# Performance work log

Measured on AMD Instinct MI355X. Metric: run time of the kernel, lower is better.

## Reference

```python
import jax, jax.numpy as jnp
import numpy as np

B, N, U, H = 4, 4096, 256, 4
NEG_PAD = -(2.0 ** 32) + 1.0  # paddings value from torch code


def setup_inputs() -> dict:
    key = jax.random.key(0)
    k1, k2, k3, k4 = jax.random.split(key, 4)
    return {
        "x": jax.random.normal(k1, (B, N, U), dtype=jnp.float32),
        "input_mask": jnp.zeros((B, N), dtype=bool),
        "Wq": jax.random.normal(k2, (U, U), dtype=jnp.float32) * 0.02,
        "Wk": jax.random.normal(k3, (U, U), dtype=jnp.float32) * 0.02,
        "Wv": jax.random.normal(k4, (U, U), dtype=jnp.float32) * 0.02,
    }


def reference(x, input_mask, Wq, Wk, Wv):
    b, n, u = x.shape
    h = H
    dh = u // h
    scale = 1.0 / np.sqrt(dh).astype(np.float32)

    # nn.Linear(bias=False): y = x @ W.T ; head split via split(dim=2)+cat(dim=0)
    # == reshape (b,n,h,dh) then move head to front -> (h,b,n,dh)
    def proj(W):
        return (x @ W.T).reshape(b, n, h, dh).transpose(2, 0, 1, 3)

    Q = proj(Wq)  # (h,b,n,dh)
    K = proj(Wk)
    V = proj(Wv)

    scores = jnp.einsum('hbqd,hbkd->hbqk', Q, K) * scale  # (h,b,n,n)

    # key mask: zero-norm keys get huge negative score
    key_masks = jnp.sign(jnp.sum(jnp.abs(K), axis=-1))  # (h,b,n)
    scores = jnp.where(key_masks[:, :, None, :] == 0, NEG_PAD, scores)

    # directional mask: attention_mask[i,j] = (j > i) for FORWARD (meshgrid ij,
    # sw_col=i, sw_row=j, greater(sw_row, sw_col)); adder kills mask==False
    idx = jnp.arange(n)
    dir_mask = idx[None, :] > idx[:, None]  # (n,n) strict upper triangle
    scores = scores + (1.0 - dir_mask.astype(scores.dtype)) * -10000.0

    attn = jax.nn.softmax(scores, axis=-1)

    # post-softmax query mask
    query_masks = jnp.sign(jnp.sum(jnp.abs(Q), axis=-1))  # (h,b,n)
    attn = attn * query_masks[..., None]

    # dropout p=0.0 -> identity
    out = jnp.einsum('hbqk,hbkd->hbqd', attn, V)  # (h,b,n,dh)
    # recombine heads: split(dim=0)+cat(dim=2) inverse -> (b,n,u)
    out = out.transpose(1, 2, 0, 3).reshape(b, n, u)

    # output value masking with ~input_mask
    out = out * (~input_mask)[..., None].astype(out.dtype)
    return out
```

## Files before the change

kernel.cpp:

```cpp
#include <hip/hip_runtime.h>
#include <hip/hip_bf16.h>
#include <stdint.h>


#define BB 4
#define NNQ 4096
#define UU 256
#define DHE 64
#define NPAIR 16
#define QBLK 128
#define KVB 128
#define NT (NNQ / KVB)
#define BIAS2 (-14426.950408889634f)
#define QSCALE 0.1803368801111244f

typedef __attribute__((ext_vector_type(8))) short bf16x8;
typedef __attribute__((ext_vector_type(4))) float f32x4;
typedef __attribute__((ext_vector_type(16))) float f32x16;
typedef unsigned short u16;
typedef unsigned int u32;

typedef __attribute__((address_space(3))) void lds_t;
typedef const __attribute__((address_space(1))) void glb_t;

__device__ __forceinline__ u16 f2bf(float f) {
    union { float f; unsigned u; } v; v.f = f;
    unsigned r = v.u + 0x7fffu + ((v.u >> 16) & 1u);
    return (u16)(r >> 16);
}

__device__ __forceinline__ float bf2f(u16 h) {
    union { unsigned u; float f; } v; v.u = ((unsigned)h) << 16;
    return v.f;
}

__device__ __forceinline__ bf16x8 load_cvt8(const float* p) {
    const float4* q = (const float4*)p;
    float4 a = q[0], b = q[1];
    bf16x8 r;
    r[0] = (short)f2bf(a.x); r[1] = (short)f2bf(a.y);
    r[2] = (short)f2bf(a.z); r[3] = (short)f2bf(a.w);
    r[4] = (short)f2bf(b.x); r[5] = (short)f2bf(b.y);
    r[6] = (short)f2bf(b.z); r[7] = (short)f2bf(b.w);
    return r;
}

__device__ __forceinline__ void gload16(const void* g, void* l) {
    __builtin_amdgcn_global_load_lds((glb_t*)g, (lds_t*)l, 16, 0, 0);
}

__device__ __forceinline__ float exp2_hw(float x) {
    float r;
    asm("v_exp_f32 %0, %1" : "=v"(r) : "v"(x));
    return r;
}

__device__ __forceinline__ float max3_hw(float a, float b, float c) {
    float r;
    asm("v_max3_f32 %0, %1, %2, %3" : "=v"(r) : "v"(a), "v"(b), "v"(c));
    return r;
}

__device__ __forceinline__ u32 cvt_pk_bf16(float a, float b) {
    u32 r;
    asm("v_cvt_pk_bf16_f32 %0, %1, %2" : "=v"(r) : "v"(a), "v"(b));
    return r;
}

__device__ __forceinline__ void pswap(u32& a, u32& b) {
    asm volatile("v_permlane32_swap_b32 %0, %1" : "+v"(a), "+v"(b));
}

__global__ __launch_bounds__(256) void cvt_kernel(
    const float* __restrict__ x, const float* __restrict__ Wq,
    const float* __restrict__ Wk, const float* __restrict__ Wv,
    u16* __restrict__ xb, u16* __restrict__ Wb)
{
    const int bx = blockIdx.x;
    if (bx < 2048) {
        const int i = (bx * 256 + threadIdx.x) * 8;
        *(bf16x8*)&xb[i] = load_cvt8(&x[i]);
    } else {
        const int zz = (bx - 2048) >> 5;
        const float* src = (zz == 0) ? Wq : (zz == 1) ? Wk : Wv;
        const int i = ((((bx - 2048) & 31) * 256) + threadIdx.x) * 8;
        *(bf16x8*)&Wb[zz * 65536 + i] = load_cvt8(&src[i]);
    }
}

__global__ __launch_bounds__(256) void proj_kernel(
    const u16* __restrict__ xb, const u16* __restrict__ Wb,
    u16* __restrict__ Qb, u16* __restrict__ Kb, u16* __restrict__ Vt)
{
    __shared__ __align__(16) u16 xbuf[64 * 256];

    const int tid = threadIdx.x;
    const int l = tid & 63;
    const int w = tid >> 6;
    const int l15 = l & 15;
    const int g = l >> 4;
    const int g8 = g * 8;
    const int z = blockIdx.y;
    const u16* W = Wb + (size_t)z * 65536;
    const int mbase = blockIdx.x * 64;

#pragma unroll
    for (int i = 0; i < 8; i++) {
        int D = tid * 16 + i * 4096;
        int S = D ^ (((D >> 9) & 7) << 4);
        gload16(xb + (size_t)mbase * UU + (S >> 1), xbuf + (D >> 1));
    }

    f32x4 acc[4][4];
#pragma unroll
    for (int mt = 0; mt < 4; mt++)
#pragma unroll
        for (int j = 0; j < 4; j++) acc[mt][j] = (f32x4){0.f, 0.f, 0.f, 0.f};

    __syncthreads();

#pragma unroll
    for (int kb = 0; kb < UU; kb += 32) {
        bf16x8 wf[4];
#pragma unroll
        for (int j = 0; j < 4; j++)
            wf[j] = *(const bf16x8*)&W[(size_t)(w * 64 + j * 16 + l15) * UU + kb + g8];
        bf16x8 af[4];
#pragma unroll
        for (int mt = 0; mt < 4; mt++) {
            int row = mt * 16 + l15;
            int A = row * 512 + (kb + g8) * 2;
            A ^= (row & 7) << 4;
            af[mt] = *(const bf16x8*)((const char*)xbuf + A);
        }
#pragma unroll
        for (int mt = 0; mt < 4; mt++)
#pragma unroll
            for (int j = 0; j < 4; j++)
                acc[mt][j] = __builtin_amdgcn_mfma_f32_16x16x32_bf16(af[mt], wf[j], acc[mt][j], 0, 0, 0);
    }

    __syncthreads();
    u16* vt = xbuf;
    const float scale = (z == 0) ? QSCALE : 1.0f;
#pragma unroll
    for (int mt = 0; mt < 4; mt++)
#pragma unroll
        for (int j = 0; j < 4; j++)
#pragma unroll
            for (int r = 0; r < 4; r++)
                vt[w * 4096 + (mt * 16 + g * 4 + r) * 64 + j * 16 + l15] =
                    f2bf(acc[mt][j][r] * scale);
    __syncthreads();

    const int bq = mbase >> 12;
    const int nbase = mbase & (NNQ - 1);
    if (z < 2) {
        u16* dst = (z == 0) ? Qb : Kb;
        const int row = tid >> 2, c16 = (tid & 3) * 16;
#pragma unroll
        for (int h = 0; h < 4; h++) {
            const int pair = h * BB + bq;
            uint4 v0 = *(const uint4*)&vt[h * 4096 + row * 64 + c16];
            uint4 v1 = *(const uint4*)&vt[h * 4096 + row * 64 + c16 + 8];
            uint4* outp = (uint4*)&dst[((size_t)pair * NNQ + nbase + row) * DHE + c16];
            outp[0] = v0; outp[1] = v1;
        }
    } else {
        const int d = tid >> 2, qq = tid & 3;
#pragma unroll
        for (int h = 0; h < 4; h++) {
            const int pair = h * BB + bq;
            u16 vals[16];
#pragma unroll
            for (int e = 0; e < 16; e++) vals[e] = vt[h * 4096 + (qq * 16 + e) * 64 + d];
            unsigned uu0[8];
#pragma unroll
            for (int e = 0; e < 8; e++)
                uu0[e] = (unsigned)vals[2 * e] | ((unsigned)vals[2 * e + 1] << 16);
            uint4* outp = (uint4*)&Vt[((size_t)(pair * DHE + d)) * NNQ + nbase + qq * 16];
            outp[0] = (uint4){uu0[0], uu0[1], uu0[2], uu0[3]};
            outp[1] = (uint4){uu0[4], uu0[5], uu0[6], uu0[7]};
        }
    }
}

__device__ __forceinline__ void stage_kv(u16* kd, u16* vd,
                                         const u16* Kp, const u16* Vp,
                                         int t, int tid)
{
#pragma unroll
    for (int i = 0; i < 2; i++) {
        int off_b = tid * 16 + i * 8192;
        int ks = off_b ^ (((off_b >> 7) & 7) << 4);
        gload16(Kp + (size_t)t * (KVB * DHE) + (ks >> 1), kd + tid * 8 + i * 4096);
        int vs = off_b ^ (((off_b >> 8) & 15) << 4);
        int d = vs >> 8;
        int c = (vs & 255) >> 1;
        gload16(Vp + (size_t)d * NNQ + t * KVB + c, vd + tid * 8 + i * 4096);
    }
}

__global__ __launch_bounds__(512, 4) void attn_kernel(
    const u16* __restrict__ Qb, const u16* __restrict__ Kb,
    const u16* __restrict__ Vt, float* __restrict__ out)
{
    __shared__ __align__(16) u16 kbuf[2][KVB * DHE];
    __shared__ __align__(16) u16 vbuf[2][DHE * KVB];
    __shared__ float mls[4][2][64];

    const int tid = threadIdx.x;
    const int l = tid & 63;
    const int w = tid >> 6;
    const int wq = w & 3;
    const int wk = w >> 2;
    const int l31 = l & 31;
    const int hi = l >> 5;
    const int hi8 = hi * 8;

    const int b = blockIdx.x;
    const int pair = (b & 7) | ((b >> 8) << 3);
    int b3 = (b >> 3) & 31;
    if (b >= 256) b3 = 31 - b3;
    const int qi = b3;
    const int qb = qi * QBLK;
    const int t0 = qi;

    const u16* Kp = Kb + (size_t)pair * NNQ * DHE;
    const u16* Vp = Vt + (size_t)pair * DHE * NNQ;

    stage_kv(kbuf[0], vbuf[0], Kp, Vp, t0, tid);

    const int wrow = qb + wq * 32;
    const int iq = wrow + l31;
    bf16x8 qf[4];
#pragma unroll
    for (int ds = 0; ds < 4; ds++)
        qf[ds] = *(const bf16x8*)&Qb[((size_t)pair * NNQ + iq) * DHE + ds * 16 + hi8];

    f32x16 oaccT[2];
#pragma unroll
    for (int dg = 0; dg < 2; dg++)
#pragma unroll
        for (int r = 0; r < 16; r++) oaccT[dg][r] = 0.f;
    float mrow = -1e30f;
    float lrow = 0.f;

    int cur = 0;
    for (int t = t0; t < NT; ++t) {
        __syncthreads();
        if (t + 1 < NT) stage_kv(kbuf[cur ^ 1], vbuf[cur ^ 1], Kp, Vp, t + 1, tid);

        const u16* kb_ = kbuf[cur];
        const u16* vb_ = vbuf[cur];

        f32x16 sT[2];
#pragma unroll
        for (int kg = 0; kg < 2; kg++)
#pragma unroll
            for (int r = 0; r < 16; r++) sT[kg][r] = 0.f;

        __builtin_amdgcn_s_setprio(1);
#pragma unroll
        for (int kg = 0; kg < 2; kg++)
#pragma unroll
            for (int ds = 0; ds < 4; ds++) {
                int e = (wk * 64 + kg * 32 + l31) * DHE + ds * 16 + hi8;
                e ^= ((e >> 6) & 7) << 3;
                bf16x8 kf = *(const bf16x8*)&kb_[e];
                sT[kg] = __builtin_amdgcn_mfma_f32_32x32x16_bf16(kf, qf[ds], sT[kg], 0, 0, 0);
            }
        __builtin_amdgcn_s_setprio(0);

        if (t == qi) {
#pragma unroll
            for (int kg = 0; kg < 2; kg++)
#pragma unroll
                for (int r = 0; r < 16; r++) {
                    int j = t * KVB + wk * 64 + kg * 32 + (r & 3) + 8 * (r >> 2) + 4 * hi;
                    if (j <= iq) sT[kg][r] += BIAS2;
                }
        }

        {
            float pmk[2];
#pragma unroll
            for (int kg = 0; kg < 2; kg++) {
                float v0 = max3_hw(sT[kg][0], sT[kg][1], sT[kg][2]);
                float v1 = max3_hw(sT[kg][3], sT[kg][4], sT[kg][5]);
                float v2 = max3_hw(sT[kg][6], sT[kg][7], sT[kg][8]);
                float v3 = max3_hw(sT[kg][9], sT[kg][10], sT[kg][11]);
                float v4 = max3_hw(sT[kg][12], sT[kg][13], sT[kg][14]);
                pmk[kg] = max3_hw(max3_hw(v0, v1, v2), fmaxf(v3, v4), sT[kg][15]);
            }
            float pm = fmaxf(pmk[0], pmk[1]);
            pm = fmaxf(pm, __shfl_xor(pm, 32));
            if (!__all(pm <= mrow + 8.0f)) {
                float mn = fmaxf(mrow, pm);
                float f = exp2_hw(mrow - mn);
                mrow = mn;
                lrow *= f;
                oaccT[0] *= f;
                oaccT[1] *= f;
            }
            float rs = 0.f;
#pragma unroll
            for (int kg = 0; kg < 2; kg++) {
#pragma unroll
                for (int r = 0; r < 16; r++)
                    sT[kg][r] = exp2_hw(sT[kg][r] - mrow);
                float s0 = (sT[kg][0] + sT[kg][1]) + (sT[kg][2] + sT[kg][3]);
                float s1 = (sT[kg][4] + sT[kg][5]) + (sT[kg][6] + sT[kg][7]);
                float s2 = (sT[kg][8] + sT[kg][9]) + (sT[kg][10] + sT[kg][11]);
                float s3 = (sT[kg][12] + sT[kg][13]) + (sT[kg][14] + sT[kg][15]);
                rs += (s0 + s1) + (s2 + s3);
            }
            rs += __shfl_xor(rs, 32);
            lrow += rs;
        }

        __builtin_amdgcn_s_setprio(1);
#pragma unroll
        for (int kg = 0; kg < 2; kg++) {
            u32 wv[8];
#pragma unroll
            for (int i = 0; i < 8; i++)
                wv[i] = cvt_pk_bf16(sT[kg][2 * i], sT[kg][2 * i + 1]);
            pswap(wv[0], wv[2]); pswap(wv[1], wv[3]);
            pswap(wv[4], wv[6]); pswap(wv[5], wv[7]);
#pragma unroll
            for (int ks = 0; ks < 2; ks++) {
                union { uint4 u; bf16x8 v; } pk;
                pk.u = (uint4){wv[ks * 4 + 0], wv[ks * 4 + 1],
                               wv[ks * 4 + 2], wv[ks * 4 + 3]};
                const int ksg = kg * 2 + ks;
#pragma unroll
                for (int dg = 0; dg < 2; dg++) {
                    int e = (dg * 32 + l31) * KVB + wk * 64 + ksg * 16 + hi8;
                    e ^= ((e >> 7) & 15) << 3;
                    bf16x8 vf = *(const bf16x8*)&vb_[e];
                    oaccT[dg] = __builtin_amdgcn_mfma_f32_32x32x16_bf16(vf, pk.v, oaccT[dg], 0, 0, 0);
                }
            }
        }
        __builtin_amdgcn_s_setprio(0);
        cur ^= 1;
    }

    __syncthreads();
    float* mb = (float*)&kbuf[0][0];
    if (wk == 1) {
        float* base = mb + wq * 2048;
#pragma unroll
        for (int dg = 0; dg < 2; dg++)
#pragma unroll
            for (int r = 0; r < 16; r++)
                base[(dg * 16 + r) * 64 + l] = oaccT[dg][r];
        mls[wq][0][l] = mrow;
        mls[wq][1][l] = lrow;
    }
    __syncthreads();
    if (wk == 0) {
        const float m1 = mls[wq][0][l];
        const float l1 = mls[wq][1][l];
        const float mn = fmaxf(mrow, m1);
        float f0 = exp2_hw(mrow - mn);
        float f1 = exp2_hw(m1 - mn);
        const float inv = 1.0f / (lrow * f0 + l1 * f1);
        f0 *= inv; f1 *= inv;
        const float* base = mb + wq * 2048;
        const int hh = pair >> 2, bb2 = pair & 3;
        float* op = &out[((size_t)(bb2 * NNQ + iq)) * UU + hh * DHE];
#pragma unroll
        for (int dg = 0; dg < 2; dg++)
#pragma unroll
            for (int rg = 0; rg < 4; rg++) {
                float vv[4];
#pragma unroll
                for (int q4 = 0; q4 < 4; q4++) {
                    int r = rg * 4 + q4;
                    vv[q4] = oaccT[dg][r] * f0 + base[(dg * 16 + r) * 64 + l] * f1;
                }
                *(float4*)&op[dg * 32 + rg * 8 + hi * 4] =
                    (float4){vv[0], vv[1], vv[2], vv[3]};
            }
    }
}

__global__ __launch_bounds__(256) void fixA_kernel(
    const u16* __restrict__ Qb, const u16* __restrict__ Kb,
    const u16* __restrict__ Vt, float* __restrict__ part)
{
    __shared__ float qs[DHE];
    __shared__ float pls[256];
    __shared__ float red[256];
    __shared__ float r4[8];

    const int tid = threadIdx.x;
    const int wv = tid >> 6;
    const int pair = blockIdx.x;
    const int sl = blockIdx.y;

    if (tid < 8) {
        bf16x8 v = *(const bf16x8*)&Qb[((size_t)pair * NNQ + (NNQ - 1)) * DHE + tid * 8];
#pragma unroll
        for (int e = 0; e < 8; e++) qs[tid * 8 + e] = bf2f((u16)v[e]);
    }
    __syncthreads();

    const int j = sl * 256 + tid;
    const u16* kr = Kb + ((size_t)pair * NNQ + j) * DHE;
    float acc = 0.f;
#pragma unroll
    for (int i = 0; i < 8; i++) {
        bf16x8 kv = *(const bf16x8*)&kr[i * 8];
#pragma unroll
        for (int e = 0; e < 8; e++) acc += qs[i * 8 + e] * bf2f((u16)kv[e]);
    }

    float m = acc;
#pragma unroll
    for (int d2 = 1; d2 < 64; d2 <<= 1) m = fmaxf(m, __shfl_xor(m, d2));
    if ((tid & 63) == 0) r4[wv] = m;
    __syncthreads();
    const float gm = fmaxf(fmaxf(r4[0], r4[1]), fmaxf(r4[2], r4[3]));

    const float p = exp2_hw(acc - gm);
    pls[tid] = p;
    float s = p;
#pragma unroll
    for (int d2 = 1; d2 < 64; d2 <<= 1) s += __shfl_xor(s, d2);
    if ((tid & 63) == 0) r4[4 + wv] = s;
    __syncthreads();
    const float gs = (r4[4] + r4[5]) + (r4[6] + r4[7]);

    const int d = tid & 63;
    const int qq = tid >> 6;
    const u16* vrow = Vt + ((size_t)pair * DHE + d) * NNQ + sl * 256 + qq * 64;
    float o = 0.f;
#pragma unroll
    for (int jj = 0; jj < 64; jj += 8) {
        bf16x8 vvv = *(const bf16x8*)&vrow[jj];
#pragma unroll
        for (int e = 0; e < 8; e++) o += pls[qq * 64 + jj + e] * bf2f((u16)vvv[e]);
    }
    red[tid] = o;
    __syncthreads();
    if (tid < 64) {
        float oo = (red[tid] + red[tid + 64]) + (red[tid + 128] + red[tid + 192]);
        float* pp = part + ((size_t)pair * 16 + sl) * 66;
        if (tid == 0) { pp[0] = gm; pp[1] = gs; }
        pp[2 + tid] = oo;
    }
}

__global__ __launch_bounds__(64) void fixB_kernel(
    const float* __restrict__ part, float* __restrict__ out)
{
    const int pair = blockIdx.x;
    const int d = threadIdx.x;
    float gm = -1e30f;
#pragma unroll
    for (int i = 0; i < 16; i++)
        gm = fmaxf(gm, part[((size_t)pair * 16 + i) * 66]);
    float gs = 0.f, od = 0.f;
#pragma unroll
    for (int i = 0; i < 16; i++) {
        const float* pp = &part[((size_t)pair * 16 + i) * 66];
        float wgt = exp2_hw(pp[0] - gm);
        gs += pp[1] * wgt;
        od += pp[2 + d] * wgt;
    }
    const int hh = pair >> 2, bb2 = pair & 3;
    out[((size_t)(bb2 * NNQ + (NNQ - 1))) * UU + hh * DHE + d] = od / gs;
}

extern "C" void kernel_launch(void* const* d_in, const int* in_sizes, int n_in,
                              void* d_out, int out_size, void* d_ws, size_t ws_size,
                              hipStream_t stream)
{
    const float* x  = (const float*)d_in[0];
    const float* Wq = (const float*)d_in[2];
    const float* Wk = (const float*)d_in[3];
    const float* Wv = (const float*)d_in[4];
    float* out = (float*)d_out;

    u16* Qb = (u16*)d_ws;
    u16* Kb = Qb + (size_t)NPAIR * NNQ * DHE;
    u16* Vt = Kb + (size_t)NPAIR * NNQ * DHE;
    float* part = (float*)(Vt + (size_t)NPAIR * DHE * NNQ);

    u16* Wb = (u16*)d_out;
    u16* xb = (u16*)d_out + 262144;

    cvt_kernel<<<2144, 256, 0, stream>>>(x, Wq, Wk, Wv, xb, Wb);

    dim3 pgrid(256, 3);
    proj_kernel<<<pgrid, 256, 0, stream>>>(xb, Wb, Qb, Kb, Vt);

    attn_kernel<<<512, 512, 0, stream>>>(Qb, Kb, Vt, out);

    dim3 fgrid(16, 16);
    fixA_kernel<<<fgrid, 256, 0, stream>>>(Qb, Kb, Vt, part);
    fixB_kernel<<<16, 64, 0, stream>>>(part, out);
}
```

Before: 96.28 us.

## Split long causal query blocks across two workgroups and fuse x conversion into projection

The attention work is rebalanced. Query blocks 0-15 have the longest key ranges, so each is split into two key-range halves handled by different workgroups. Those workgroups write bf16 partial outputs with their max and sum, and a new merge kernel combines them. The second-half workgroups also process the short query blocks 16-31 directly, so every workgroup does about 17 tiles. Separately, the x-to-bf16 conversion is folded into proj_kernel's LDS fill, which removes a pass over x. The cost is an extra launch, partial-buffer traffic, and bf16 rounding of the partial outputs.

```diff
diff --git a/kernel.cpp b/kernel.cpp
--- a/kernel.cpp
+++ b/kernel.cpp
@@ -10,7 +10,7 @@
 #define NPAIR 16
 #define QBLK 128
 #define KVB 128
-#define NT (NNQ / KVB)
+#define NT 32
 #define BIAS2 (-14426.950408889634f)
 #define QSCALE 0.1803368801111244f
 
@@ -71,25 +71,18 @@
     asm volatile("v_permlane32_swap_b32 %0, %1" : "+v"(a), "+v"(b));
 }
 
-__global__ __launch_bounds__(256) void cvt_kernel(
-    const float* __restrict__ x, const float* __restrict__ Wq,
-    const float* __restrict__ Wk, const float* __restrict__ Wv,
-    u16* __restrict__ xb, u16* __restrict__ Wb)
-{
-    const int bx = blockIdx.x;
-    if (bx < 2048) {
-        const int i = (bx * 256 + threadIdx.x) * 8;
-        *(bf16x8*)&xb[i] = load_cvt8(&x[i]);
-    } else {
-        const int zz = (bx - 2048) >> 5;
-        const float* src = (zz == 0) ? Wq : (zz == 1) ? Wk : Wv;
-        const int i = ((((bx - 2048) & 31) * 256) + threadIdx.x) * 8;
-        *(bf16x8*)&Wb[zz * 65536 + i] = load_cvt8(&src[i]);
-    }
+__global__ __launch_bounds__(256) void cvtw_kernel(
+    const float* __restrict__ Wq, const float* __restrict__ Wk,
+    const float* __restrict__ Wv, u16* __restrict__ Wb)
+{
+    const int z = blockIdx.y;
+    const float* src = (z == 0) ? Wq : (z == 1) ? Wk : Wv;
+    const int i = (blockIdx.x * 256 + threadIdx.x) * 8;
+    *(bf16x8*)&Wb[z * 65536 + i] = load_cvt8(&src[i]);
 }
 
 __global__ __launch_bounds__(256) void proj_kernel(
-    const u16* __restrict__ xb, const u16* __restrict__ Wb,
+    const float* __restrict__ x, const u16* __restrict__ Wb,
     u16* __restrict__ Qb, u16* __restrict__ Kb, u16* __restrict__ Vt)
 {
     __shared__ __align__(16) u16 xbuf[64 * 256];
@@ -104,11 +97,16 @@
     const u16* W = Wb + (size_t)z * 65536;
     const int mbase = blockIdx.x * 64;
 
-#pragma unroll
-    for (int i = 0; i < 8; i++) {
-        int D = tid * 16 + i * 4096;
-        int S = D ^ (((D >> 9) & 7) << 4);
-        gload16(xb + (size_t)mbase * UU + (S >> 1), xbuf + (D >> 1));
+    const float4* xs = (const float4*)&x[(size_t)mbase * UU];
+#pragma unroll
+    for (int i = 0; i < 16; i++) {
+        int idx4 = i * 256 + tid;
+        float4 v = xs[idx4];
+        u32 p0 = cvt_pk_bf16(v.x, v.y);
+        u32 p1 = cvt_pk_bf16(v.z, v.w);
+        int Lin = idx4 * 8;
+        int Dst = Lin ^ (((Lin >> 9) & 7) << 4);
+        *(uint2*)((char*)xbuf + Dst) = (uint2){p0, p1};
     }
 
     f32x4 acc[4][4];
@@ -203,7 +201,9 @@
 
 __global__ __launch_bounds__(512, 4) void attn_kernel(
     const u16* __restrict__ Qb, const u16* __restrict__ Kb,
-    const u16* __restrict__ Vt, float* __restrict__ out)
+    const u16* __restrict__ Vt, float* __restrict__ out,
+    float2* __restrict__ pm_a, u16* __restrict__ po_a,
+    float2* __restrict__ pm_b, u16* __restrict__ po_b)
 {
     __shared__ __align__(16) u16 kbuf[2][KVB * DHE];
     __shared__ __align__(16) u16 vbuf[2][DHE * KVB];
@@ -220,171 +220,272 @@
 
     const int b = blockIdx.x;
     const int pair = (b & 7) | ((b >> 8) << 3);
-    int b3 = (b >> 3) & 31;
-    if (b >= 256) b3 = 31 - b3;
-    const int qi = b3;
-    const int qb = qi * QBLK;
-    const int t0 = qi;
+    const int s = (b >> 3) & 31;
+    const int x = s & 15;
+    const int half = s >> 4;
 
     const u16* Kp = Kb + (size_t)pair * NNQ * DHE;
     const u16* Vp = Vt + (size_t)pair * DHE * NNQ;
 
-    stage_kv(kbuf[0], vbuf[0], Kp, Vp, t0, tid);
-
-    const int wrow = qb + wq * 32;
-    const int iq = wrow + l31;
-    bf16x8 qf[4];
-#pragma unroll
-    for (int ds = 0; ds < 4; ds++)
-        qf[ds] = *(const bf16x8*)&Qb[((size_t)pair * NNQ + iq) * DHE + ds * 16 + hi8];
-
     f32x16 oaccT[2];
-#pragma unroll
-    for (int dg = 0; dg < 2; dg++)
-#pragma unroll
-        for (int r = 0; r < 16; r++) oaccT[dg][r] = 0.f;
-    float mrow = -1e30f;
-    float lrow = 0.f;
-
-    int cur = 0;
-    for (int t = t0; t < NT; ++t) {
-        __syncthreads();
-        if (t + 1 < NT) stage_kv(kbuf[cur ^ 1], vbuf[cur ^ 1], Kp, Vp, t + 1, tid);
-
-        const u16* kb_ = kbuf[cur];
-        const u16* vb_ = vbuf[cur];
-
-        f32x16 sT[2];
-#pragma unroll
-        for (int kg = 0; kg < 2; kg++)
-#pragma unroll
-            for (int r = 0; r < 16; r++) sT[kg][r] = 0.f;
-
-        __builtin_amdgcn_s_setprio(1);
-#pragma unroll
-        for (int kg = 0; kg < 2; kg++)
-#pragma unroll
-            for (int ds = 0; ds < 4; ds++) {
-                int e = (wk * 64 + kg * 32 + l31) * DHE + ds * 16 + hi8;
-                e ^= ((e >> 6) & 7) << 3;
-                bf16x8 kf = *(const bf16x8*)&kb_[e];
-                sT[kg] = __builtin_amdgcn_mfma_f32_32x32x16_bf16(kf, qf[ds], sT[kg], 0, 0, 0);
+    float mrow, lrow;
+
+    auto reset = [&]() {
+#pragma unroll
+        for (int dg = 0; dg < 2; dg++)
+#pragma unroll
+            for (int r = 0; r < 16; r++) oaccT[dg][r] = 0.f;
+        mrow = -1e30f; lrow = 0.f;
+    };
+
+    auto flash_pass = [&](int qi, int ta, int tb, bool masked) {
+        if (ta >= tb) return;
+        const int iq = qi * QBLK + wq * 32 + l31;
+        bf16x8 qf[4];
+#pragma unroll
+        for (int ds = 0; ds < 4; ds++)
+            qf[ds] = *(const bf16x8*)&Qb[((size_t)pair * NNQ + iq) * DHE + ds * 16 + hi8];
+
+        stage_kv(kbuf[0], vbuf[0], Kp, Vp, ta, tid);
+        int cur = 0;
+        for (int t = ta; t < tb; ++t) {
+            __syncthreads();
+            if (t + 1 < tb) stage_kv(kbuf[cur ^ 1], vbuf[cur ^ 1], Kp, Vp, t + 1, tid);
+
+            const u16* kb_ = kbuf[cur];
+            const u16* vb_ = vbuf[cur];
+
+            f32x16 sT[2];
+#pragma unroll
+            for (int kg = 0; kg < 2; kg++)
+#pragma unroll
+                for (int r = 0; r < 16; r++) sT[kg][r] = 0.f;
+
+            __builtin_amdgcn_s_setprio(1);
+#pragma unroll
+            for (int kg = 0; kg < 2; kg++)
+#pragma unroll
+                for (int ds = 0; ds < 4; ds++) {
+                    int e = (wk * 64 + kg * 32 + l31) * DHE + ds * 16 + hi8;
+                    e ^= ((e >> 6) & 7) << 3;
+                    bf16x8 kf = *(const bf16x8*)&kb_[e];
+                    sT[kg] = __builtin_amdgcn_mfma_f32_32x32x16_bf16(kf, qf[ds], sT[kg], 0, 0, 0);
+                }
+            __builtin_amdgcn_s_setprio(0);
+
+            if (masked && t == qi) {
+#pragma unroll
+                for (int kg = 0; kg < 2; kg++)
+#pragma unroll
+                    for (int r = 0; r < 16; r++) {
+                        int j = t * KVB + wk * 64 + kg * 32 + (r & 3) + 8 * (r >> 2) + 4 * hi;
+                        if (j <= iq) sT[kg][r] += BIAS2;
+                    }
             }
-        __builtin_amdgcn_s_setprio(0);
-
-        if (t == qi) {
-#pragma unroll
-            for (int kg = 0; kg < 2; kg++)
-#pragma unroll
-                for (int r = 0; r < 16; r++) {
-                    int j = t * KVB + wk * 64 + kg * 32 + (r & 3) + 8 * (r >> 2) + 4 * hi;
-                    if (j <= iq) sT[kg][r] += BIAS2;
+
+            {
+                float pmk[2];
+#pragma unroll
+                for (int kg = 0; kg < 2; kg++) {
+                    float v0 = max3_hw(sT[kg][0], sT[kg][1], sT[kg][2]);
+                    float v1 = max3_hw(sT[kg][3], sT[kg][4], sT[kg][5]);
+                    float v2 = max3_hw(sT[kg][6], sT[kg][7], sT[kg][8]);
+                    float v3 = max3_hw(sT[kg][9], sT[kg][10], sT[kg][11]);
+                    float v4 = max3_hw(sT[kg][12], sT[kg][13], sT[kg][14]);
+                    pmk[kg] = max3_hw(max3_hw(v0, v1, v2), fmaxf(v3, v4), sT[kg][15]);
                 }
-        }
-
-        {
-            float pmk[2];
+                float pm = fmaxf(pmk[0], pmk[1]);
+                pm = fmaxf(pm, __shfl_xor(pm, 32));
+                if (!__all(pm <= mrow + 8.0f)) {
+                    float mn = fmaxf(mrow, pm);
+                    float f = exp2_hw(mrow - mn);
+                    mrow = mn;
+                    lrow *= f;
+                    oaccT[0] *= f;
+                    oaccT[1] *= f;
+                }
+                float rs = 0.f;
+#pragma unroll
+                for (int kg = 0; kg < 2; kg++) {
+#pragma unroll
+                    for (int r = 0; r < 16; r++)
+                        sT[kg][r] = exp2_hw(sT[kg][r] - mrow);
+                    float s0 = (sT[kg][0] + sT[kg][1]) + (sT[kg][2] + sT[kg][3]);
+                    float s1 = (sT[kg][4] + sT[kg][5]) + (sT[kg][6] + sT[kg][7]);
+                    float s2 = (sT[kg][8] + sT[kg][9]) + (sT[kg][10] + sT[kg][11]);
+                    float s3 = (sT[kg][12] + sT[kg][13]) + (sT[kg][14] + sT[kg][15]);
+                    rs += (s0 + s1) + (s2 + s3);
+                }
+                rs += __shfl_xor(rs, 32);
+                lrow += rs;
+            }
+
+            __builtin_amdgcn_s_setprio(1);
 #pragma unroll
             for (int kg = 0; kg < 2; kg++) {
-                float v0 = max3_hw(sT[kg][0], sT[kg][1], sT[kg][2]);
-                float v1 = max3_hw(sT[kg][3], sT[kg][4], sT[kg][5]);
-                float v2 = max3_hw(sT[kg][6], sT[kg][7], sT[kg][8]);
-                float v3 = max3_hw(sT[kg][9], sT[kg][10], sT[kg][11]);
-                float v4 = max3_hw(sT[kg][12], sT[kg][13], sT[kg][14]);
-                pmk[kg] = max3_hw(max3_hw(v0, v1, v2), fmaxf(v3, v4), sT[kg][15]);
-            }
-            float pm = fmaxf(pmk[0], pmk[1]);
-            pm = fmaxf(pm, __shfl_xor(pm, 32));
-            if (!__all(pm <= mrow + 8.0f)) {
-                float mn = fmaxf(mrow, pm);
-                float f = exp2_hw(mrow - mn);
-                mrow = mn;
-                lrow *= f;
-                oaccT[0] *= f;
-                oaccT[1] *= f;
-            }
-            float rs = 0.f;
-#pragma unroll
-            for (int kg = 0; kg < 2; kg++) {
-#pragma unroll
-                for (int r = 0; r < 16; r++)
-                    sT[kg][r] = exp2_hw(sT[kg][r] - mrow);
-                float s0 = (sT[kg][0] + sT[kg][1]) + (sT[kg][2] + sT[kg][3]);
-                float s1 = (sT[kg][4] + sT[kg][5]) + (sT[kg][6] + sT[kg][7]);
-                float s2 = (sT[kg][8] + sT[kg][9]) + (sT[kg][10] + sT[kg][11]);
-                float s3 = (sT[kg][12] + sT[kg][13]) + (sT[kg][14] + sT[kg][15]);
-                rs += (s0 + s1) + (s2 + s3);
-            }
-            rs += __shfl_xor(rs, 32);
-            lrow += rs;
-        }
-
-        __builtin_amdgcn_s_setprio(1);
-#pragma unroll
-        for (int kg = 0; kg < 2; kg++) {
-            u32 wv[8];
-#pragma unroll
-            for (int i = 0; i < 8; i++)
-                wv[i] = cvt_pk_bf16(sT[kg][2 * i], sT[kg][2 * i + 1]);
-            pswap(wv[0], wv[2]); pswap(wv[1], wv[3]);
-            pswap(wv[4], wv[6]); pswap(wv[5], wv[7]);
-#pragma unroll
-            for (int ks = 0; ks < 2; ks++) {
-                union { uint4 u; bf16x8 v; } pk;
-                pk.u = (uint4){wv[ks * 4 + 0], wv[ks * 4 + 1],
-                               wv[ks * 4 + 2], wv[ks * 4 + 3]};
-                const int ksg = kg * 2 + ks;
-#pragma unroll
-                for (int dg = 0; dg < 2; dg++) {
-                    int e = (dg * 32 + l31) * KVB + wk * 64 + ksg * 16 + hi8;
-                    e ^= ((e >> 7) & 15) << 3;
-                    bf16x8 vf = *(const bf16x8*)&vb_[e];
-                    oaccT[dg] = __builtin_amdgcn_mfma_f32_32x32x16_bf16(vf, pk.v, oaccT[dg], 0, 0, 0);
+                u32 wv[8];
+#pragma unroll
+                for (int i = 0; i < 8; i++)
+                    wv[i] = cvt_pk_bf16(sT[kg][2 * i], sT[kg][2 * i + 1]);
+                pswap(wv[0], wv[2]); pswap(wv[1], wv[3]);
+                pswap(wv[4], wv[6]); pswap(wv[5], wv[7]);
+#pragma unroll
+                for (int ks = 0; ks < 2; ks++) {
+                    union { uint4 u; bf16x8 v; } pk;
+                    pk.u = (uint4){wv[ks * 4 + 0], wv[ks * 4 + 1],
+                                   wv[ks * 4 + 2], wv[ks * 4 + 3]};
+                    const int ksg = kg * 2 + ks;
+#pragma unroll
+                    for (int dg = 0; dg < 2; dg++) {
+                        int e = (dg * 32 + l31) * KVB + wk * 64 + ksg * 16 + hi8;
+                        e ^= ((e >> 7) & 15) << 3;
+                        bf16x8 vf = *(const bf16x8*)&vb_[e];
+                        oaccT[dg] = __builtin_amdgcn_mfma_f32_32x32x16_bf16(vf, pk.v, oaccT[dg], 0, 0, 0);
+                    }
                 }
             }
-        }
-        __builtin_amdgcn_s_setprio(0);
-        cur ^= 1;
-    }
-
-    __syncthreads();
-    float* mb = (float*)&kbuf[0][0];
-    if (wk == 1) {
-        float* base = mb + wq * 2048;
-#pragma unroll
-        for (int dg = 0; dg < 2; dg++)
-#pragma unroll
-            for (int r = 0; r < 16; r++)
-                base[(dg * 16 + r) * 64 + l] = oaccT[dg][r];
-        mls[wq][0][l] = mrow;
-        mls[wq][1][l] = lrow;
-    }
-    __syncthreads();
-    if (wk == 0) {
-        const float m1 = mls[wq][0][l];
-        const float l1 = mls[wq][1][l];
-        const float mn = fmaxf(mrow, m1);
-        float f0 = exp2_hw(mrow - mn);
-        float f1 = exp2_hw(m1 - mn);
-        const float inv = 1.0f / (lrow * f0 + l1 * f1);
-        f0 *= inv; f1 *= inv;
-        const float* base = mb + wq * 2048;
-        const int hh = pair >> 2, bb2 = pair & 3;
-        float* op = &out[((size_t)(bb2 * NNQ + iq)) * UU + hh * DHE];
-#pragma unroll
-        for (int dg = 0; dg < 2; dg++)
-#pragma unroll
-            for (int rg = 0; rg < 4; rg++) {
-                float vv[4];
-#pragma unroll
-                for (int q4 = 0; q4 < 4; q4++) {
-                    int r = rg * 4 + q4;
-                    vv[q4] = oaccT[dg][r] * f0 + base[(dg * 16 + r) * 64 + l] * f1;
+            __builtin_amdgcn_s_setprio(0);
+            cur ^= 1;
+        }
+    };
+
+    auto epi_partial = [&](float2* pm, u16* po) {
+        __syncthreads();
+        float* mb = (float*)&kbuf[0][0];
+        if (wk == 1) {
+            float* basep = mb + wq * 2048;
+#pragma unroll
+            for (int dg = 0; dg < 2; dg++)
+#pragma unroll
+                for (int r = 0; r < 16; r++)
+                    basep[(dg * 16 + r) * 64 + l] = oaccT[dg][r];
+            mls[wq][0][l] = mrow;
+            mls[wq][1][l] = lrow;
+        }
+        __syncthreads();
+        if (wk == 0) {
+            const float m1 = mls[wq][0][l];
+            const float l1 = mls[wq][1][l];
+            const float mn = fmaxf(mrow, m1);
+            const float f0 = exp2_hw(mrow - mn);
+            const float f1 = exp2_hw(m1 - mn);
+            const float lc = lrow * f0 + l1 * f1;
+            const float invl = (lc > 0.f) ? 1.0f / lc : 0.f;
+            const float* basep = mb + wq * 2048;
+            const int row = wq * 32 + l31;
+            const size_t rb = (size_t)((pair * 16 + x) * 128 + row);
+            if (hi == 0) pm[rb] = (float2){mn, lc};
+            u16* pr = po + rb * 64;
+#pragma unroll
+            for (int dg = 0; dg < 2; dg++)
+#pragma unroll
+                for (int rg = 0; rg < 4; rg++) {
+                    float vv[4];
+#pragma unroll
+                    for (int q4 = 0; q4 < 4; q4++) {
+                        int r = rg * 4 + q4;
+                        vv[q4] = (oaccT[dg][r] * f0 + basep[(dg * 16 + r) * 64 + l] * f1) * invl;
+                    }
+                    u32 plo = cvt_pk_bf16(vv[0], vv[1]);
+                    u32 phi = cvt_pk_bf16(vv[2], vv[3]);
+                    *(uint2*)&pr[dg * 32 + rg * 8 + hi * 4] = (uint2){plo, phi};
                 }
-                *(float4*)&op[dg * 32 + rg * 8 + hi * 4] =
-                    (float4){vv[0], vv[1], vv[2], vv[3]};
-            }
-    }
+        }
+        __syncthreads();
+    };
+
+    if (half == 0) {
+        reset();
+        flash_pass(x, x, x + 17, true);
+        epi_partial(pm_a, po_a);
+    } else {
+        reset();
+        flash_pass(x, x + 17, NT, false);
+        epi_partial(pm_b, po_b);
+
+        reset();
+        const int qi2 = 31 - x;
+        flash_pass(qi2, qi2, NT, true);
+
+        __syncthreads();
+        float* mb = (float*)&kbuf[0][0];
+        if (wk == 1) {
+            float* basep = mb + wq * 2048;
+#pragma unroll
+            for (int dg = 0; dg < 2; dg++)
+#pragma unroll
+                for (int r = 0; r < 16; r++)
+                    basep[(dg * 16 + r) * 64 + l] = oaccT[dg][r];
+            mls[wq][0][l] = mrow;
+            mls[wq][1][l] = lrow;
+        }
+        __syncthreads();
+        if (wk == 0) {
+            const float m1 = mls[wq][0][l];
+            const float l1 = mls[wq][1][l];
+            const float mn = fmaxf(mrow, m1);
+            float f0 = exp2_hw(mrow - mn);
+            float f1 = exp2_hw(m1 - mn);
+            const float inv = 1.0f / (lrow * f0 + l1 * f1);
+            f0 *= inv; f1 *= inv;
+            const float* basep = mb + wq * 2048;
+            const int hh = pair >> 2, bb2 = pair & 3;
+            const int n = qi2 * QBLK + wq * 32 + l31;
+            float* op = &out[((size_t)(bb2 * NNQ + n)) * UU + hh * DHE];
+#pragma unroll
+            for (int dg = 0; dg < 2; dg++)
+#pragma unroll
+                for (int rg = 0; rg < 4; rg++) {
+                    float vv[4];
+#pragma unroll
+                    for (int q4 = 0; q4 < 4; q4++) {
+                        int r = rg * 4 + q4;
+                        vv[q4] = oaccT[dg][r] * f0 + basep[(dg * 16 + r) * 64 + l] * f1;
+                    }
+                    *(float4*)&op[dg * 32 + rg * 8 + hi * 4] =
+                        (float4){vv[0], vv[1], vv[2], vv[3]};
+                }
+        }
+    }
+}
+
+__global__ __launch_bounds__(512) void mergeq_kernel(
+    const float2* __restrict__ pm_a, const u16* __restrict__ po_a,
+    const float2* __restrict__ pm_b, const u16* __restrict__ po_b,
+    float* __restrict__ out)
+{
+    const int gi = blockIdx.x;
+    const int pair = gi >> 4;
+    const int x = gi & 15;
+    const int tid = threadIdx.x;
+    const int row = tid >> 2;
+    const int dq = (tid & 3) * 16;
+    const size_t rb = (size_t)gi * 128 + row;
+
+    const float2 A = pm_a[rb];
+    const float2 Bv = pm_b[rb];
+    const float mn = fmaxf(A.x, Bv.x);
+    float fa = A.y * exp2_hw(A.x - mn);
+    float fb = Bv.y * exp2_hw(Bv.x - mn);
+    const float inv = 1.0f / (fa + fb);
+    fa *= inv; fb *= inv;
+
+    const u16* pa = po_a + rb * 64 + dq;
+    const u16* pb = po_b + rb * 64 + dq;
+    bf16x8 va0 = *(const bf16x8*)&pa[0], va1 = *(const bf16x8*)&pa[8];
+    bf16x8 vb0 = *(const bf16x8*)&pb[0], vb1 = *(const bf16x8*)&pb[8];
+    float ov[16];
+#pragma unroll
+    for (int e = 0; e < 8; e++) {
+        ov[e] = bf2f((u16)va0[e]) * fa + bf2f((u16)vb0[e]) * fb;
+        ov[8 + e] = bf2f((u16)va1[e]) * fa + bf2f((u16)vb1[e]) * fb;
+    }
+    const int hh = pair >> 2, bb2 = pair & 3;
+    const int n = x * 128 + row;
+    float* op = &out[((size_t)(bb2 * NNQ + n)) * UU + hh * DHE + dq];
+#pragma unroll
+    for (int i = 0; i < 4; i++)
+        *(float4*)&op[i * 4] = (float4){ov[4 * i], ov[4 * i + 1], ov[4 * i + 2], ov[4 * i + 3]};
 }
 
 __global__ __launch_bounds__(256) void fixA_kernel(
@@ -485,20 +586,27 @@
     const float* Wv = (const float*)d_in[4];
     float* out = (float*)d_out;
 
+    const size_t QSZ = (size_t)NPAIR * NNQ * DHE;
     u16* Qb = (u16*)d_ws;
-    u16* Kb = Qb + (size_t)NPAIR * NNQ * DHE;
-    u16* Vt = Kb + (size_t)NPAIR * NNQ * DHE;
-    float* part = (float*)(Vt + (size_t)NPAIR * DHE * NNQ);
+    u16* Kb = Qb + QSZ;
+    u16* Vt = Kb + QSZ;
+    float* part = (float*)(Vt + QSZ);
+    float2* pm_a = (float2*)(part + 16896);
+    float2* pm_b = pm_a + 32768;
+    u16* po_a = (u16*)(pm_b + 32768);
+    u16* po_b = po_a + (size_t)32768 * 64;
 
     u16* Wb = (u16*)d_out;
-    u16* xb = (u16*)d_out + 262144;
-
-    cvt_kernel<<<2144, 256, 0, stream>>>(x, Wq, Wk, Wv, xb, Wb);
+
+    dim3 cgrid(32, 3);
+    cvtw_kernel<<<cgrid, 256, 0, stream>>>(Wq, Wk, Wv, Wb);
 
     dim3 pgrid(256, 3);
-    proj_kernel<<<pgrid, 256, 0, stream>>>(xb, Wb, Qb, Kb, Vt);
-
-    attn_kernel<<<512, 512, 0, stream>>>(Qb, Kb, Vt, out);
+    proj_kernel<<<pgrid, 256, 0, stream>>>(x, Wb, Qb, Kb, Vt);
+
+    attn_kernel<<<512, 512, 0, stream>>>(Qb, Kb, Vt, out, pm_a, po_a, pm_b, po_b);
+
+    mergeq_kernel<<<256, 512, 0, stream>>>(pm_a, po_a, pm_b, po_b, out);
 
     dim3 fgrid(16, 16);
     fixA_kernel<<<fgrid, 256, 0, stream>>>(Qb, Kb, Vt, part);
```

New measurement: 95.79 us. Within noise of the previous version (-0.5%).
